# Kernel tuning notes

Hardware: AMD Instinct MI355X
Metric: run time of the kernel (lower is better)

## Reference

```python
import jax, jax.numpy as jnp
import numpy as np

DIM = 512
HEADS = 8
DIM_HEAD = 64
HIDDEN = HEADS * DIM_HEAD  # 512
B, N = 16, 4096
EPS = 1e-5


def setup_inputs() -> dict:
    key = jax.random.key(0)
    k1, k2, k3 = jax.random.split(key, 3)
    x = jax.random.normal(k1, (B, DIM, N), dtype=jnp.float32)
    # Conv1d kernel-size-1 weights stored as [out_ch, in_ch]
    w_qkv = jax.random.normal(k2, (3 * HIDDEN, DIM), dtype=jnp.float32) / np.sqrt(DIM)
    w_out = jax.random.normal(k3, (DIM, HIDDEN), dtype=jnp.float32) / np.sqrt(HIDDEN)
    b_out = jnp.zeros((DIM,), dtype=jnp.float32)
    g_out = jnp.ones((DIM,), dtype=jnp.float32)  # channel LayerNorm gamma
    return {"x": x, "w_qkv": w_qkv, "w_out": w_out, "b_out": b_out, "g_out": g_out}


def reference(x, w_qkv, w_out, b_out, g_out):
    b, c, n = x.shape
    scale = DIM_HEAD ** (-0.5)
    # 1x1 conv projection to q,k,v: [b, 3*hidden, n]
    qkv = jnp.einsum('bcn,oc->bon', x, w_qkv)
    q, k, v = jnp.split(qkv, 3, axis=1)
    rs = lambda t: t.reshape(b, HEADS, DIM_HEAD, n)  # b (m d) n -> b m d n
    q, k, v = rs(q), rs(k), rs(v)
    q = jax.nn.softmax(q, axis=2) * scale  # softmax over head-dim d
    k = jax.nn.softmax(k, axis=3)          # softmax over sequence n
    # context: k v^T outer-product summed over sequence -> [b, m, d, d]
    context = jnp.einsum('bmin,bmjn->bmij', k, v)
    # apply context to queries -> [b, m, d, n]
    out = jnp.einsum('bmij,bmin->bmjn', context, q)
    out = out.reshape(b, HIDDEN, n)  # b m d n -> b (m d) n
    # output 1x1 conv with bias
    out = jnp.einsum('bcn,oc->bon', out, w_out) + b_out[None, :, None]
    # channel LayerNorm (gamma-only, biased variance over channel axis)
    mean = out.mean(axis=1, keepdims=True)
    var = out.var(axis=1, keepdims=True)
    return (out - mean) * jax.lax.rsqrt(var + EPS) * g_out[None, :, None]
```

## Files before the change

kernel.cpp:

```cpp
#include <hip/hip_runtime.h>

#define NB 16
#define CDIM 512
#define NHEAD 8
#define DHEAD 64
#define NSEQ 4096
#define O3 1536

typedef __attribute__((ext_vector_type(8))) short short8;
typedef __attribute__((ext_vector_type(4))) float f32x4;
typedef __attribute__((ext_vector_type(4))) unsigned u32x4;
typedef __attribute__((ext_vector_type(2))) unsigned u32x2;
typedef __attribute__((ext_vector_type(4))) float fvec4;

__device__ __forceinline__ float bf2f(unsigned short u){
  union { unsigned u; float f; } v; v.u = ((unsigned)u) << 16; return v.f;
}
__device__ __forceinline__ unsigned short f2bf(float f){
  union { float f; unsigned u; } v; v.f = f;
  unsigned r = v.u + 0x7fffu + ((v.u >> 16) & 1u);
  return (unsigned short)(r >> 16);
}
__device__ __forceinline__ unsigned pack2(float a, float b){
  return (unsigned)f2bf(a) | ((unsigned)f2bf(b) << 16);
}
__device__ __forceinline__ void gld_lds16(const void* g, void* l){
  __builtin_amdgcn_global_load_lds(
      (const __attribute__((address_space(1))) unsigned*)g,
      (__attribute__((address_space(3))) unsigned*)l, 16, 0, 0);
}

__global__ __launch_bounds__(256) void k_conv_w(const float* __restrict__ w,
                                                unsigned short* __restrict__ o){
  int i = (blockIdx.x*256 + threadIdx.x)*4;
  fvec4 v = *(const fvec4*)(w + i);
  u32x2 p; p[0] = pack2(v[0], v[1]); p[1] = pack2(v[2], v[3]);
  *(u32x2*)(o + i) = p;
}

__global__ __launch_bounds__(256) void k_transpose_x(const float* __restrict__ x,
                                                     unsigned short* __restrict__ xT){
  __shared__ unsigned short tile[64][65];
  int b = blockIdx.z, c0 = blockIdx.y*64, n0 = blockIdx.x*64;
  int t = threadIdx.x;
  const float* xb = x + ((size_t)b*CDIM + c0)*NSEQ + n0;
  #pragma unroll
  for (int i=0;i<4;i++){
    int idx = t + i*256;
    int r = idx>>4, c4 = (idx&15)*4;
    fvec4 v = *(const fvec4*)(xb + (size_t)r*NSEQ + c4);
    tile[r][c4]   = f2bf(v[0]);
    tile[r][c4+1] = f2bf(v[1]);
    tile[r][c4+2] = f2bf(v[2]);
    tile[r][c4+3] = f2bf(v[3]);
  }
  __syncthreads();
  unsigned short* ob = xT + ((size_t)b*NSEQ + n0)*CDIM + c0;
  #pragma unroll
  for (int i=0;i<2;i++){
    int chunk = t + i*256;
    int r = chunk>>3, c8 = (chunk&7)*8;
    u32x4 p;
    #pragma unroll
    for (int k=0;k<4;k++)
      p[k] = (unsigned)tile[c8+2*k][r] | ((unsigned)tile[c8+2*k+1][r] << 16);
    *(u32x4*)(ob + (size_t)r*CDIM + c8) = p;
  }
}

__global__ __launch_bounds__(256) void k_gemm_kv(const unsigned short* __restrict__ A,
                                                 const unsigned short* __restrict__ Bt,
                                                 unsigned short* __restrict__ KV){
  __shared__ unsigned short As[2][128*32];
  __shared__ unsigned short Bs[2][128*32];
  int b = blockIdx.z;
  int n0 = blockIdx.x*128, o0 = blockIdx.y*128;
  const unsigned short* Bb = Bt + (size_t)b*NSEQ*CDIM;
  unsigned short* Cb = KV + (size_t)b*1024*NSEQ;
  int t = threadIdx.x, w = t>>6, l = t&63;
  int lr = l&15, kq = (l>>4)*8;
  int wr = (w>>1)*64, wc = (w&1)*64;
  f32x4 acc[4][4];
  #pragma unroll
  for (int mi=0;mi<4;mi++)
    #pragma unroll
    for (int ni=0;ni<4;ni++) acc[mi][ni] = (f32x4){0.f,0.f,0.f,0.f};
  for (int k0=0;k0<CDIM;k0+=64){
    #pragma unroll
    for (int h=0;h<2;++h){
      #pragma unroll
      for (int it=0;it<2;++it){
        int chunk = it*256 + t;
        int row = chunk>>2, kc = (chunk&3)*8;
        gld_lds16(A  + (size_t)(o0+row)*CDIM + k0 + h*32 + kc, (char*)As[h] + (size_t)chunk*16);
        gld_lds16(Bb + (size_t)(n0+row)*CDIM + k0 + h*32 + kc, (char*)Bs[h] + (size_t)chunk*16);
      }
    }
    __syncthreads();
    #pragma unroll
    for (int h=0;h<2;++h){
      short8 af[4], bfv[4];
      #pragma unroll
      for (int mi=0;mi<4;mi++) af[mi]  = *(const short8*)&As[h][(wr + mi*16 + lr)*32 + kq];
      #pragma unroll
      for (int ni=0;ni<4;ni++) bfv[ni] = *(const short8*)&Bs[h][(wc + ni*16 + lr)*32 + kq];
      #pragma unroll
      for (int mi=0;mi<4;mi++)
        #pragma unroll
        for (int ni=0;ni<4;ni++)
          acc[mi][ni] = __builtin_amdgcn_mfma_f32_16x16x32_bf16(af[mi], bfv[ni], acc[mi][ni], 0, 0, 0);
    }
    __syncthreads();
  }
  #pragma unroll
  for (int mi=0;mi<4;mi++)
    #pragma unroll
    for (int ni=0;ni<4;ni++)
      #pragma unroll
      for (int r=0;r<4;r++){
        int row = o0 + wr + mi*16 + (l>>4)*4 + r;
        int col = n0 + wc + ni*16 + lr;
        Cb[(size_t)row*NSEQ + col] = f2bf(acc[mi][ni][r]);
      }
}

#define TS 136
__global__ __launch_bounds__(256) void k_gemm_q(const unsigned short* __restrict__ A,
                                                const unsigned short* __restrict__ Bt,
                                                unsigned short* __restrict__ qsmT){
  __shared__ unsigned short smem[128*128];
  int b = blockIdx.z;
  int n0 = blockIdx.x*128, o0 = blockIdx.y*128;
  const unsigned short* Bb = Bt + (size_t)b*NSEQ*CDIM;
  int t = threadIdx.x, w = t>>6, l = t&63;
  int lr = l&15, kq = (l>>4)*8;
  int wr = (w>>1)*64, wc = (w&1)*64;
  f32x4 acc[4][4];
  #pragma unroll
  for (int mi=0;mi<4;mi++)
    #pragma unroll
    for (int ni=0;ni<4;ni++) acc[mi][ni] = (f32x4){0.f,0.f,0.f,0.f};
  for (int k0=0;k0<CDIM;k0+=64){
    #pragma unroll
    for (int h=0;h<2;++h){
      unsigned short* Ash = smem + h*4096;
      unsigned short* Bsh = smem + 8192 + h*4096;
      #pragma unroll
      for (int it=0;it<2;++it){
        int chunk = it*256 + t;
        int row = chunk>>2, kc = (chunk&3)*8;
        gld_lds16(A  + (size_t)(o0+row)*CDIM + k0 + h*32 + kc, (char*)Ash + (size_t)chunk*16);
        gld_lds16(Bb + (size_t)(n0+row)*CDIM + k0 + h*32 + kc, (char*)Bsh + (size_t)chunk*16);
      }
    }
    __syncthreads();
    #pragma unroll
    for (int h=0;h<2;++h){
      const unsigned short* Ash = smem + h*4096;
      const unsigned short* Bsh = smem + 8192 + h*4096;
      short8 af[4], bfv[4];
      #pragma unroll
      for (int mi=0;mi<4;mi++) af[mi]  = *(const short8*)&Ash[(wr + mi*16 + lr)*32 + kq];
      #pragma unroll
      for (int ni=0;ni<4;ni++) bfv[ni] = *(const short8*)&Bsh[(wc + ni*16 + lr)*32 + kq];
      #pragma unroll
      for (int mi=0;mi<4;mi++)
        #pragma unroll
        for (int ni=0;ni<4;ni++)
          acc[mi][ni] = __builtin_amdgcn_mfma_f32_16x16x32_bf16(af[mi], bfv[ni], acc[mi][ni], 0, 0, 0);
    }
    __syncthreads();
  }
  unsigned pk[4][4][2];
  #pragma unroll
  for (int ni=0;ni<4;ni++){
    float mx = -1e30f;
    #pragma unroll
    for (int mi=0;mi<4;mi++)
      #pragma unroll
      for (int r=0;r<4;r++) mx = fmaxf(mx, acc[mi][ni][r]);
    mx = fmaxf(mx, __shfl_xor(mx, 16, 64));
    mx = fmaxf(mx, __shfl_xor(mx, 32, 64));
    float s = 0.f;
    #pragma unroll
    for (int mi=0;mi<4;mi++)
      #pragma unroll
      for (int r=0;r<4;r++){
        float p = __expf(acc[mi][ni][r] - mx);
        acc[mi][ni][r] = p; s += p;
      }
    s += __shfl_xor(s, 16, 64);
    s += __shfl_xor(s, 32, 64);
    float inv = 0.125f / s;
    #pragma unroll
    for (int mi=0;mi<4;mi++){
      pk[mi][ni][0] = pack2(acc[mi][ni][0]*inv, acc[mi][ni][1]*inv);
      pk[mi][ni][1] = pack2(acc[mi][ni][2]*inv, acc[mi][ni][3]*inv);
    }
  }
  #pragma unroll
  for (int ck=0;ck<2;++ck){
    if ((w&1) == ck){
      #pragma unroll
      for (int mi=0;mi<4;mi++)
        #pragma unroll
        for (int ni=0;ni<4;ni++){
          int idx = (ni*16 + lr)*TS + wr + mi*16 + (l>>4)*4;
          u32x2 p; p[0] = pk[mi][ni][0]; p[1] = pk[mi][ni][1];
          *(u32x2*)&smem[idx] = p;
        }
    }
    __syncthreads();
    int col = t>>2, rs = (t&3)*32;
    unsigned short* dst = qsmT + ((size_t)b*NSEQ + n0 + ck*64 + col)*CDIM + o0 + rs;
    #pragma unroll
    for (int j=0;j<4;++j)
      *(u32x4*)(dst + j*8) = *(const u32x4*)&smem[col*TS + rs + j*8];
    __syncthreads();
  }
}

__global__ __launch_bounds__(256) void k_context(const unsigned short* __restrict__ KV,
                                                 float* __restrict__ ctx4,
                                                 float* __restrict__ sump){
  __shared__ unsigned short Vs[64*64];
  int m = blockIdx.x, b = blockIdx.y, ch = blockIdx.z;
  int t = threadIdx.x, w = t>>6, l = t&63;
  int lr = l&15, kq = (l>>4)*8;
  const unsigned short* kbase = KV + ((size_t)b*1024 + m*64)*NSEQ;
  const unsigned short* vbase = KV + ((size_t)b*1024 + 512 + m*64)*NSEQ;
  int irow = w*16 + lr;
  int sub = l>>4;
  int nbeg = ch*1024;
  float rsum = 0.f;
  f32x4 acc[4];
  #pragma unroll
  for (int jf=0;jf<4;++jf) acc[jf] = (f32x4){0.f,0.f,0.f,0.f};
  for (int n0=nbeg;n0<nbeg+1024;n0+=64){
    #pragma unroll
    for (int it=0;it<2;++it){
      int chunk = it*256 + t;
      int row = chunk>>3, kc = (chunk&7)*8;
      gld_lds16(vbase + (size_t)row*NSEQ + n0 + kc, (char*)Vs + (size_t)chunk*16);
    }
    __syncthreads();
    #pragma unroll
    for (int kk=0;kk<2;++kk){
      u32x4 kraw = *(const u32x4*)(kbase + (size_t)irow*NSEQ + n0 + kk*32 + kq);
      short8 af;
      #pragma unroll
      for (int c=0;c<4;++c){
        unsigned u = kraw[c];
        float f0 = __expf(bf2f((unsigned short)u));
        float f1 = __expf(bf2f((unsigned short)(u>>16)));
        rsum += f0 + f1;
        af[c*2]   = (short)f2bf(f0);
        af[c*2+1] = (short)f2bf(f1);
      }
      #pragma unroll
      for (int jf=0;jf<4;++jf){
        short8 bv = *(const short8*)&Vs[(jf*16+lr)*64 + kk*32 + kq];
        acc[jf] = __builtin_amdgcn_mfma_f32_16x16x32_bf16(af, bv, acc[jf], 0, 0, 0);
      }
    }
    __syncthreads();
  }
  rsum += __shfl_xor(rsum, 16, 64);
  rsum += __shfl_xor(rsum, 32, 64);
  size_t sbase = (((size_t)ch*NB + b)*NHEAD + m)*64;
  if (sub == 0) sump[sbase + irow] = rsum;
  float* cb = ctx4 + (((size_t)ch*NB + b)*NHEAD + m)*4096;
  #pragma unroll
  for (int jf=0;jf<4;++jf)
    #pragma unroll
    for (int r=0;r<4;++r){
      int i = w*16 + (l>>4)*4 + r;
      int j = jf*16 + lr;
      cb[i*64 + j] = acc[jf][r];
    }
}

__global__ __launch_bounds__(256) void k_weff(const float* __restrict__ ctx4,
                                              const float* __restrict__ sump,
                                              const float* __restrict__ wout,
                                              unsigned short* __restrict__ weff){
  __shared__ float cs[64][65];
  __shared__ float invZ[64];
  int m = blockIdx.x, b = blockIdx.y, z = blockIdx.z;
  int t = threadIdx.x, w = t>>6, l = t&63;
  const size_t chs = (size_t)NB*NHEAD*4096;
  const size_t sts = (size_t)NB*NHEAD*64;
  size_t sb = ((size_t)b*NHEAD + m)*64;
  if (t < 64){
    float Z = sump[sb + t] + sump[sb + sts + t]
            + sump[sb + 2*sts + t] + sump[sb + 3*sts + t];
    invZ[t] = 1.f/Z;
  }
  __syncthreads();
  const float* cb = ctx4 + ((size_t)b*NHEAD + m)*4096;
  for (int idx=t; idx<4096; idx+=256){
    int i = idx>>6;
    cs[i][idx&63] = (cb[idx] + cb[idx+chs] + cb[idx+2*chs] + cb[idx+3*chs]) * invZ[i];
  }
  __syncthreads();
  for (int oo=0;oo<32;++oo){
    int o = z*128 + w*32 + oo;
    float acc = 0.f;
    #pragma unroll
    for (int j=0;j<64;++j) acc += wout[(size_t)o*CDIM + m*64 + j] * cs[l][j];
    weff[((size_t)b*CDIM + o)*CDIM + m*64 + l] = f2bf(acc);
  }
}

__global__ __launch_bounds__(512) void k_out_ln(const unsigned short* __restrict__ Weff,
                                                const unsigned short* __restrict__ QT,
                                                const float* __restrict__ bias,
                                                const float* __restrict__ g,
                                                float* __restrict__ out){
  __shared__ unsigned short As[512*32];
  __shared__ unsigned short Bs[128*32];
  __shared__ float lnS[128], lnS2[128];
  int b = blockIdx.y, n0 = blockIdx.x*128;
  const unsigned short* Ab = Weff + (size_t)b*CDIM*CDIM;
  const unsigned short* Bb = QT + ((size_t)b*NSEQ + n0)*CDIM;
  int t = threadIdx.x, w = t>>6, l = t&63;
  int lr = l&15, kq = (l>>4)*8;
  f32x4 acc[4][8];
  #pragma unroll
  for (int mi=0;mi<4;mi++)
    #pragma unroll
    for (int ni=0;ni<8;ni++) acc[mi][ni] = (f32x4){0.f,0.f,0.f,0.f};
  for (int k0=0;k0<CDIM;k0+=32){
    #pragma unroll
    for (int it=0;it<4;++it){
      int chunk = it*512 + t;
      int row = chunk>>2, kc = (chunk&3)*8;
      gld_lds16(Ab + (size_t)row*CDIM + k0 + kc, (char*)As + (size_t)chunk*16);
    }
    {
      int row = t>>2, kc = (t&3)*8;
      gld_lds16(Bb + (size_t)row*CDIM + k0 + kc, (char*)Bs + (size_t)t*16);
    }
    __syncthreads();
    short8 af[4], bfv[8];
    #pragma unroll
    for (int mi=0;mi<4;mi++) af[mi]  = *(const short8*)&As[(w*64 + mi*16 + lr)*32 + kq];
    #pragma unroll
    for (int ni=0;ni<8;ni++) bfv[ni] = *(const short8*)&Bs[(ni*16 + lr)*32 + kq];
    #pragma unroll
    for (int mi=0;mi<4;mi++)
      #pragma unroll
      for (int ni=0;ni<8;ni++)
        acc[mi][ni] = __builtin_amdgcn_mfma_f32_16x16x32_bf16(af[mi], bfv[ni], acc[mi][ni], 0, 0, 0);
    __syncthreads();
  }
  if (t < 128){ lnS[t] = 0.f; lnS2[t] = 0.f; }
  __syncthreads();
  float ps[8], ps2[8];
  #pragma unroll
  for (int ni=0;ni<8;ni++){ ps[ni]=0.f; ps2[ni]=0.f; }
  #pragma unroll
  for (int mi=0;mi<4;mi++)
    #pragma unroll
    for (int r=0;r<4;r++){
      int row = w*64 + mi*16 + (l>>4)*4 + r;
      float bb = bias[row];
      #pragma unroll
      for (int ni=0;ni<8;ni++){
        float v = acc[mi][ni][r] + bb;
        acc[mi][ni][r] = v;
        ps[ni] += v; ps2[ni] += v*v;
      }
    }
  #pragma unroll
  for (int ni=0;ni<8;ni++){
    ps[ni]  += __shfl_xor(ps[ni], 16, 64);  ps[ni]  += __shfl_xor(ps[ni], 32, 64);
    ps2[ni] += __shfl_xor(ps2[ni], 16, 64); ps2[ni] += __shfl_xor(ps2[ni], 32, 64);
  }
  if ((l>>4) == 0){
    #pragma unroll
    for (int ni=0;ni<8;ni++){
      atomicAdd(&lnS[ni*16+lr],  ps[ni]);
      atomicAdd(&lnS2[ni*16+lr], ps2[ni]);
    }
  }
  __syncthreads();
  if (t < 128){
    float mean = lnS[t]*(1.f/512.f);
    float var  = lnS2[t]*(1.f/512.f) - mean*mean;
    lnS[t] = mean; lnS2[t] = rsqrtf(var + 1e-5f);
  }
  __syncthreads();
  float* ob = out + (size_t)b*CDIM*NSEQ + n0;
  #pragma unroll
  for (int ni=0;ni<8;ni++){
    int col = ni*16 + lr;
    float mean = lnS[col], rstd = lnS2[col];
    #pragma unroll
    for (int mi=0;mi<4;mi++)
      #pragma unroll
      for (int r=0;r<4;r++){
        int row = w*64 + mi*16 + (l>>4)*4 + r;
        ob[(size_t)row*NSEQ + col] = (acc[mi][ni][r] - mean)*rstd*g[row];
      }
  }
}

extern "C" void kernel_launch(void* const* d_in, const int* in_sizes, int n_in,
                              void* d_out, int out_size, void* d_ws, size_t ws_size,
                              hipStream_t stream){
  const float* x     = (const float*)d_in[0];
  const float* w_qkv = (const float*)d_in[1];
  const float* w_out = (const float*)d_in[2];
  const float* b_out = (const float*)d_in[3];
  const float* g_out = (const float*)d_in[4];
  float* out = (float*)d_out;
  char* ws = (char*)d_ws;

  size_t off = 0;
  unsigned short* wq_bf = (unsigned short*)(ws + off); off += (size_t)O3*CDIM*2;
  char* xT_region = ws + off;                          off += (size_t)NB*NSEQ*CDIM*2;
  unsigned short* qkv_kv = (unsigned short*)(ws + off); off += (size_t)NB*1024*NSEQ*2;
  unsigned short* qsmT   = (unsigned short*)(ws + off); off += (size_t)NB*NSEQ*CDIM*2;
  if (off > ws_size) return;
  unsigned short* xT = (unsigned short*)xT_region;
  float* sump = (float*)(xT_region);
  float* ctx4 = (float*)(xT_region + (1<<20));
  unsigned short* weff = (unsigned short*)(xT_region + (16<<20));

  k_conv_w     <<<O3*CDIM/1024, 256, 0, stream>>>(w_qkv, wq_bf);
  k_transpose_x<<<dim3(NSEQ/64, CDIM/64, NB), 256, 0, stream>>>(x, xT);
  k_gemm_kv    <<<dim3(NSEQ/128, 8, NB), 256, 0, stream>>>(wq_bf + (size_t)512*CDIM, xT, qkv_kv);
  k_gemm_q     <<<dim3(NSEQ/128, 4, NB), 256, 0, stream>>>(wq_bf, xT, qsmT);
  k_context    <<<dim3(NHEAD, NB, 4), 256, 0, stream>>>(qkv_kv, ctx4, sump);
  k_weff       <<<dim3(NHEAD, NB, 4), 256, 0, stream>>>(ctx4, sump, w_out, weff);
  k_out_ln     <<<dim3(NSEQ/128, NB), 512, 0, stream>>>(weff, qsmT, b_out, g_out, out);
}
```

Baseline: 373.4 us.

## Fuse K/V projection GEMM with exp and context accumulation per head

Merges the K/V projection GEMM and the context kernel into one kernel. Each block computes a 128-column slab of K and V for one head, applies exp and row sums to K in LDS, and accumulates K·V^T with MFMA. The goal is to stop writing and re-reading the full bf16 KV tensor (about 128 MB) to global memory. In exchange the sequence is split into 8 chunks, so the reduction in k_weff grows from 4 to 8 partials. The grid is also smaller (8x8x16 = 1024 blocks), and each block runs a second MFMA phase with extra barriers.

```diff
diff --git a/kernel.cpp b/kernel.cpp
--- a/kernel.cpp
+++ b/kernel.cpp
@@ -68,60 +68,112 @@
   }
 }
 
-__global__ __launch_bounds__(256) void k_gemm_kv(const unsigned short* __restrict__ A,
-                                                 const unsigned short* __restrict__ Bt,
-                                                 unsigned short* __restrict__ KV){
-  __shared__ unsigned short As[2][128*32];
-  __shared__ unsigned short Bs[2][128*32];
-  int b = blockIdx.z;
-  int n0 = blockIdx.x*128, o0 = blockIdx.y*128;
-  const unsigned short* Bb = Bt + (size_t)b*NSEQ*CDIM;
-  unsigned short* Cb = KV + (size_t)b*1024*NSEQ;
+#define CS 136
+__global__ __launch_bounds__(256) void k_kvctx(const unsigned short* __restrict__ wq,
+                                               const unsigned short* __restrict__ Bt,
+                                               float* __restrict__ ctx8,
+                                               float* __restrict__ sump8){
+  __shared__ char lds[35072];
+  unsigned short* AsB = (unsigned short*)lds;
+  unsigned short* BsB = (unsigned short*)(lds + 16384);
+  unsigned short* Klds = (unsigned short*)lds;
+  unsigned short* Vlds = (unsigned short*)(lds + 17408);
+  float* rsumL = (float*)(lds + 34816);
+  int ch = blockIdx.x, m = blockIdx.y, b = blockIdx.z;
   int t = threadIdx.x, w = t>>6, l = t&63;
   int lr = l&15, kq = (l>>4)*8;
   int wr = (w>>1)*64, wc = (w&1)*64;
-  f32x4 acc[4][4];
-  #pragma unroll
-  for (int mi=0;mi<4;mi++)
-    #pragma unroll
-    for (int ni=0;ni<4;ni++) acc[mi][ni] = (f32x4){0.f,0.f,0.f,0.f};
-  for (int k0=0;k0<CDIM;k0+=64){
-    #pragma unroll
-    for (int h=0;h<2;++h){
-      #pragma unroll
-      for (int it=0;it<2;++it){
-        int chunk = it*256 + t;
-        int row = chunk>>2, kc = (chunk&3)*8;
-        gld_lds16(A  + (size_t)(o0+row)*CDIM + k0 + h*32 + kc, (char*)As[h] + (size_t)chunk*16);
-        gld_lds16(Bb + (size_t)(n0+row)*CDIM + k0 + h*32 + kc, (char*)Bs[h] + (size_t)chunk*16);
-      }
-    }
-    __syncthreads();
-    #pragma unroll
-    for (int h=0;h<2;++h){
-      short8 af[4], bfv[4];
-      #pragma unroll
-      for (int mi=0;mi<4;mi++) af[mi]  = *(const short8*)&As[h][(wr + mi*16 + lr)*32 + kq];
-      #pragma unroll
-      for (int ni=0;ni<4;ni++) bfv[ni] = *(const short8*)&Bs[h][(wc + ni*16 + lr)*32 + kq];
+  const unsigned short* Ak = wq + (size_t)(512  + m*64)*CDIM;
+  const unsigned short* Av = wq + (size_t)(1024 + m*64)*CDIM;
+  if (t < 64) rsumL[t] = 0.f;
+  f32x4 cacc[4];
+  #pragma unroll
+  for (int jf=0;jf<4;++jf) cacc[jf] = (f32x4){0.f,0.f,0.f,0.f};
+
+  for (int s=0;s<4;++s){
+    const unsigned short* Bb = Bt + ((size_t)b*NSEQ + ch*512 + s*128)*CDIM;
+    f32x4 acc[4][4];
+    #pragma unroll
+    for (int mi=0;mi<4;mi++)
+      #pragma unroll
+      for (int ni=0;ni<4;ni++) acc[mi][ni] = (f32x4){0.f,0.f,0.f,0.f};
+    for (int k0=0;k0<CDIM;k0+=64){
+      #pragma unroll
+      for (int h=0;h<2;++h){
+        #pragma unroll
+        for (int it=0;it<2;++it){
+          int chunk = it*256 + t;
+          int row = chunk>>2, kc = (chunk&3)*8;
+          const unsigned short* ar = (row < 64) ? (Ak + (size_t)row*CDIM)
+                                                : (Av + (size_t)(row-64)*CDIM);
+          gld_lds16(ar + k0 + h*32 + kc, lds + (size_t)(h*512+chunk)*16);
+          gld_lds16(Bb + (size_t)row*CDIM + k0 + h*32 + kc,
+                    lds + 16384 + (size_t)(h*512+chunk)*16);
+        }
+      }
+      __syncthreads();
+      #pragma unroll
+      for (int h=0;h<2;++h){
+        short8 af[4], bfv[4];
+        #pragma unroll
+        for (int mi=0;mi<4;mi++) af[mi]  = *(const short8*)&AsB[h*4096 + (wr + mi*16 + lr)*32 + kq];
+        #pragma unroll
+        for (int ni=0;ni<4;ni++) bfv[ni] = *(const short8*)&BsB[h*4096 + (wc + ni*16 + lr)*32 + kq];
+        #pragma unroll
+        for (int mi=0;mi<4;mi++)
+          #pragma unroll
+          for (int ni=0;ni<4;ni++)
+            acc[mi][ni] = __builtin_amdgcn_mfma_f32_16x16x32_bf16(af[mi], bfv[ni], acc[mi][ni], 0, 0, 0);
+      }
+      __syncthreads();
+    }
+    if (w < 2){
       #pragma unroll
       for (int mi=0;mi<4;mi++)
         #pragma unroll
-        for (int ni=0;ni<4;ni++)
-          acc[mi][ni] = __builtin_amdgcn_mfma_f32_16x16x32_bf16(af[mi], bfv[ni], acc[mi][ni], 0, 0, 0);
-    }
-    __syncthreads();
-  }
-  #pragma unroll
-  for (int mi=0;mi<4;mi++)
-    #pragma unroll
-    for (int ni=0;ni<4;ni++)
-      #pragma unroll
-      for (int r=0;r<4;r++){
-        int row = o0 + wr + mi*16 + (l>>4)*4 + r;
-        int col = n0 + wc + ni*16 + lr;
-        Cb[(size_t)row*NSEQ + col] = f2bf(acc[mi][ni][r]);
-      }
+        for (int r=0;r<4;r++){
+          int row = mi*16 + (l>>4)*4 + r;
+          float rs = 0.f;
+          #pragma unroll
+          for (int ni=0;ni<4;ni++){
+            float e = __expf(acc[mi][ni][r]);
+            rs += e;
+            Klds[row*CS + wc + ni*16 + lr] = f2bf(e);
+          }
+          rs += __shfl_xor(rs, 1, 64); rs += __shfl_xor(rs, 2, 64);
+          rs += __shfl_xor(rs, 4, 64); rs += __shfl_xor(rs, 8, 64);
+          if (lr == 0) atomicAdd(&rsumL[row], rs);
+        }
+    } else {
+      #pragma unroll
+      for (int mi=0;mi<4;mi++)
+        #pragma unroll
+        for (int r=0;r<4;r++){
+          int row = mi*16 + (l>>4)*4 + r;
+          #pragma unroll
+          for (int ni=0;ni<4;ni++)
+            Vlds[row*CS + wc + ni*16 + lr] = f2bf(acc[mi][ni][r]);
+        }
+    }
+    __syncthreads();
+    #pragma unroll
+    for (int ks=0;ks<4;++ks){
+      short8 af = *(const short8*)&Klds[(w*16 + lr)*CS + ks*32 + kq];
+      #pragma unroll
+      for (int jf=0;jf<4;++jf){
+        short8 bv = *(const short8*)&Vlds[(jf*16 + lr)*CS + ks*32 + kq];
+        cacc[jf] = __builtin_amdgcn_mfma_f32_16x16x32_bf16(af, bv, cacc[jf], 0, 0, 0);
+      }
+    }
+    __syncthreads();
+  }
+  float* cb = ctx8 + (((size_t)ch*NB + b)*NHEAD + m)*4096;
+  #pragma unroll
+  for (int jf=0;jf<4;++jf)
+    #pragma unroll
+    for (int r=0;r<4;++r)
+      cb[(w*16 + (l>>4)*4 + r)*64 + jf*16 + lr] = cacc[jf][r];
+  if (t < 64) sump8[(((size_t)ch*NB + b)*NHEAD + m)*64 + t] = rsumL[t];
 }
 
 #define TS 136
@@ -220,68 +272,8 @@
   }
 }
 
-__global__ __launch_bounds__(256) void k_context(const unsigned short* __restrict__ KV,
-                                                 float* __restrict__ ctx4,
-                                                 float* __restrict__ sump){
-  __shared__ unsigned short Vs[64*64];
-  int m = blockIdx.x, b = blockIdx.y, ch = blockIdx.z;
-  int t = threadIdx.x, w = t>>6, l = t&63;
-  int lr = l&15, kq = (l>>4)*8;
-  const unsigned short* kbase = KV + ((size_t)b*1024 + m*64)*NSEQ;
-  const unsigned short* vbase = KV + ((size_t)b*1024 + 512 + m*64)*NSEQ;
-  int irow = w*16 + lr;
-  int sub = l>>4;
-  int nbeg = ch*1024;
-  float rsum = 0.f;
-  f32x4 acc[4];
-  #pragma unroll
-  for (int jf=0;jf<4;++jf) acc[jf] = (f32x4){0.f,0.f,0.f,0.f};
-  for (int n0=nbeg;n0<nbeg+1024;n0+=64){
-    #pragma unroll
-    for (int it=0;it<2;++it){
-      int chunk = it*256 + t;
-      int row = chunk>>3, kc = (chunk&7)*8;
-      gld_lds16(vbase + (size_t)row*NSEQ + n0 + kc, (char*)Vs + (size_t)chunk*16);
-    }
-    __syncthreads();
-    #pragma unroll
-    for (int kk=0;kk<2;++kk){
-      u32x4 kraw = *(const u32x4*)(kbase + (size_t)irow*NSEQ + n0 + kk*32 + kq);
-      short8 af;
-      #pragma unroll
-      for (int c=0;c<4;++c){
-        unsigned u = kraw[c];
-        float f0 = __expf(bf2f((unsigned short)u));
-        float f1 = __expf(bf2f((unsigned short)(u>>16)));
-        rsum += f0 + f1;
-        af[c*2]   = (short)f2bf(f0);
-        af[c*2+1] = (short)f2bf(f1);
-      }
-      #pragma unroll
-      for (int jf=0;jf<4;++jf){
-        short8 bv = *(const short8*)&Vs[(jf*16+lr)*64 + kk*32 + kq];
-        acc[jf] = __builtin_amdgcn_mfma_f32_16x16x32_bf16(af, bv, acc[jf], 0, 0, 0);
-      }
-    }
-    __syncthreads();
-  }
-  rsum += __shfl_xor(rsum, 16, 64);
-  rsum += __shfl_xor(rsum, 32, 64);
-  size_t sbase = (((size_t)ch*NB + b)*NHEAD + m)*64;
-  if (sub == 0) sump[sbase + irow] = rsum;
-  float* cb = ctx4 + (((size_t)ch*NB + b)*NHEAD + m)*4096;
-  #pragma unroll
-  for (int jf=0;jf<4;++jf)
-    #pragma unroll
-    for (int r=0;r<4;++r){
-      int i = w*16 + (l>>4)*4 + r;
-      int j = jf*16 + lr;
-      cb[i*64 + j] = acc[jf][r];
-    }
-}
-
-__global__ __launch_bounds__(256) void k_weff(const float* __restrict__ ctx4,
-                                              const float* __restrict__ sump,
+__global__ __launch_bounds__(256) void k_weff(const float* __restrict__ ctx8,
+                                              const float* __restrict__ sump8,
                                               const float* __restrict__ wout,
                                               unsigned short* __restrict__ weff){
   __shared__ float cs[64][65];
@@ -292,15 +284,19 @@
   const size_t sts = (size_t)NB*NHEAD*64;
   size_t sb = ((size_t)b*NHEAD + m)*64;
   if (t < 64){
-    float Z = sump[sb + t] + sump[sb + sts + t]
-            + sump[sb + 2*sts + t] + sump[sb + 3*sts + t];
+    float Z = 0.f;
+    #pragma unroll
+    for (int c=0;c<8;++c) Z += sump8[sb + c*sts + t];
     invZ[t] = 1.f/Z;
   }
   __syncthreads();
-  const float* cb = ctx4 + ((size_t)b*NHEAD + m)*4096;
+  const float* cb = ctx8 + ((size_t)b*NHEAD + m)*4096;
   for (int idx=t; idx<4096; idx+=256){
     int i = idx>>6;
-    cs[i][idx&63] = (cb[idx] + cb[idx+chs] + cb[idx+2*chs] + cb[idx+3*chs]) * invZ[i];
+    float v = 0.f;
+    #pragma unroll
+    for (int c=0;c<8;++c) v += cb[idx + c*chs];
+    cs[i][idx&63] = v * invZ[i];
   }
   __syncthreads();
   for (int oo=0;oo<32;++oo){
@@ -419,20 +415,18 @@
 
   size_t off = 0;
   unsigned short* wq_bf = (unsigned short*)(ws + off); off += (size_t)O3*CDIM*2;
-  char* xT_region = ws + off;                          off += (size_t)NB*NSEQ*CDIM*2;
-  unsigned short* qkv_kv = (unsigned short*)(ws + off); off += (size_t)NB*1024*NSEQ*2;
-  unsigned short* qsmT   = (unsigned short*)(ws + off); off += (size_t)NB*NSEQ*CDIM*2;
+  unsigned short* xT    = (unsigned short*)(ws + off); off += (size_t)NB*NSEQ*CDIM*2;
+  char* scratch = ws + off;                            off += (size_t)NB*1024*NSEQ*2;
+  unsigned short* qsmT  = (unsigned short*)(ws + off); off += (size_t)NB*NSEQ*CDIM*2;
   if (off > ws_size) return;
-  unsigned short* xT = (unsigned short*)xT_region;
-  float* sump = (float*)(xT_region);
-  float* ctx4 = (float*)(xT_region + (1<<20));
-  unsigned short* weff = (unsigned short*)(xT_region + (16<<20));
+  float* sump8 = (float*)(scratch);
+  float* ctx8  = (float*)(scratch + (1<<20));
+  unsigned short* weff = (unsigned short*)(scratch + (20<<20));
 
   k_conv_w     <<<O3*CDIM/1024, 256, 0, stream>>>(w_qkv, wq_bf);
   k_transpose_x<<<dim3(NSEQ/64, CDIM/64, NB), 256, 0, stream>>>(x, xT);
-  k_gemm_kv    <<<dim3(NSEQ/128, 8, NB), 256, 0, stream>>>(wq_bf + (size_t)512*CDIM, xT, qkv_kv);
+  k_kvctx      <<<dim3(8, NHEAD, NB), 256, 0, stream>>>(wq_bf, xT, ctx8, sump8);
   k_gemm_q     <<<dim3(NSEQ/128, 4, NB), 256, 0, stream>>>(wq_bf, xT, qsmT);
-  k_context    <<<dim3(NHEAD, NB, 4), 256, 0, stream>>>(qkv_kv, ctx4, sump);
-  k_weff       <<<dim3(NHEAD, NB, 4), 256, 0, stream>>>(ctx4, sump, w_out, weff);
+  k_weff       <<<dim3(NHEAD, NB, 4), 256, 0, stream>>>(ctx8, sump8, w_out, weff);
   k_out_ln     <<<dim3(NSEQ/128, NB), 512, 0, stream>>>(weff, qsmT, b_out, g_out, out);
 }
```

Result: slower. 445.2 us (+19.2%).

## Double-buffer K-slices in QKV projection GEMMs to overlap loads with MFMA

Applied to the files above, without the earlier changes.

Changes the kv and q projection GEMM main loops from loading a 64-wide K chunk and then computing on it into a ping-pong pipeline over 32-wide K slices. The next slice is prefetched into the alternate LDS buffer while MFMAs run on the current one, with one barrier per step. The goal is to hide global-to-LDS latency behind compute. In exchange it doubles the number of barriers and loop iterations, and correctness relies on the async LDS load having landed before the barrier.

```diff
diff --git a/kernel.cpp b/kernel.cpp
--- a/kernel.cpp
+++ b/kernel.cpp
@@ -85,32 +85,33 @@
   for (int mi=0;mi<4;mi++)
     #pragma unroll
     for (int ni=0;ni<4;ni++) acc[mi][ni] = (f32x4){0.f,0.f,0.f,0.f};
-  for (int k0=0;k0<CDIM;k0+=64){
-    #pragma unroll
-    for (int h=0;h<2;++h){
-      #pragma unroll
-      for (int it=0;it<2;++it){
-        int chunk = it*256 + t;
-        int row = chunk>>2, kc = (chunk&3)*8;
-        gld_lds16(A  + (size_t)(o0+row)*CDIM + k0 + h*32 + kc, (char*)As[h] + (size_t)chunk*16);
-        gld_lds16(Bb + (size_t)(n0+row)*CDIM + k0 + h*32 + kc, (char*)Bs[h] + (size_t)chunk*16);
-      }
-    }
-    __syncthreads();
-    #pragma unroll
-    for (int h=0;h<2;++h){
-      short8 af[4], bfv[4];
-      #pragma unroll
-      for (int mi=0;mi<4;mi++) af[mi]  = *(const short8*)&As[h][(wr + mi*16 + lr)*32 + kq];
-      #pragma unroll
-      for (int ni=0;ni<4;ni++) bfv[ni] = *(const short8*)&Bs[h][(wc + ni*16 + lr)*32 + kq];
-      #pragma unroll
-      for (int mi=0;mi<4;mi++)
-        #pragma unroll
-        for (int ni=0;ni<4;ni++)
-          acc[mi][ni] = __builtin_amdgcn_mfma_f32_16x16x32_bf16(af[mi], bfv[ni], acc[mi][ni], 0, 0, 0);
-    }
-    __syncthreads();
+  auto STAGE = [&](int k0, int buf){
+    #pragma unroll
+    for (int it=0;it<2;++it){
+      int chunk = it*256 + t;
+      int row = chunk>>2, kc = (chunk&3)*8;
+      gld_lds16(A  + (size_t)(o0+row)*CDIM + k0 + kc, (char*)As[buf] + (size_t)chunk*16);
+      gld_lds16(Bb + (size_t)(n0+row)*CDIM + k0 + kc, (char*)Bs[buf] + (size_t)chunk*16);
+    }
+  };
+  STAGE(0, 0);
+  __syncthreads();
+  int cur = 0;
+  #pragma unroll 2
+  for (int k0=0;k0<CDIM;k0+=32){
+    if (k0+32 < CDIM) STAGE(k0+32, cur^1);
+    short8 af[4], bfv[4];
+    #pragma unroll
+    for (int mi=0;mi<4;mi++) af[mi]  = *(const short8*)&As[cur][(wr + mi*16 + lr)*32 + kq];
+    #pragma unroll
+    for (int ni=0;ni<4;ni++) bfv[ni] = *(const short8*)&Bs[cur][(wc + ni*16 + lr)*32 + kq];
+    #pragma unroll
+    for (int mi=0;mi<4;mi++)
+      #pragma unroll
+      for (int ni=0;ni<4;ni++)
+        acc[mi][ni] = __builtin_amdgcn_mfma_f32_16x16x32_bf16(af[mi], bfv[ni], acc[mi][ni], 0, 0, 0);
+    __syncthreads();
+    cur ^= 1;
   }
   #pragma unroll
   for (int mi=0;mi<4;mi++)
@@ -140,36 +141,37 @@
   for (int mi=0;mi<4;mi++)
     #pragma unroll
     for (int ni=0;ni<4;ni++) acc[mi][ni] = (f32x4){0.f,0.f,0.f,0.f};
-  for (int k0=0;k0<CDIM;k0+=64){
-    #pragma unroll
-    for (int h=0;h<2;++h){
-      unsigned short* Ash = smem + h*4096;
-      unsigned short* Bsh = smem + 8192 + h*4096;
-      #pragma unroll
-      for (int it=0;it<2;++it){
-        int chunk = it*256 + t;
-        int row = chunk>>2, kc = (chunk&3)*8;
-        gld_lds16(A  + (size_t)(o0+row)*CDIM + k0 + h*32 + kc, (char*)Ash + (size_t)chunk*16);
-        gld_lds16(Bb + (size_t)(n0+row)*CDIM + k0 + h*32 + kc, (char*)Bsh + (size_t)chunk*16);
-      }
-    }
-    __syncthreads();
-    #pragma unroll
-    for (int h=0;h<2;++h){
-      const unsigned short* Ash = smem + h*4096;
-      const unsigned short* Bsh = smem + 8192 + h*4096;
-      short8 af[4], bfv[4];
-      #pragma unroll
-      for (int mi=0;mi<4;mi++) af[mi]  = *(const short8*)&Ash[(wr + mi*16 + lr)*32 + kq];
-      #pragma unroll
-      for (int ni=0;ni<4;ni++) bfv[ni] = *(const short8*)&Bsh[(wc + ni*16 + lr)*32 + kq];
-      #pragma unroll
-      for (int mi=0;mi<4;mi++)
-        #pragma unroll
-        for (int ni=0;ni<4;ni++)
-          acc[mi][ni] = __builtin_amdgcn_mfma_f32_16x16x32_bf16(af[mi], bfv[ni], acc[mi][ni], 0, 0, 0);
-    }
-    __syncthreads();
+  auto STAGE = [&](int k0, int buf){
+    unsigned short* Ash = smem + buf*4096;
+    unsigned short* Bsh = smem + 8192 + buf*4096;
+    #pragma unroll
+    for (int it=0;it<2;++it){
+      int chunk = it*256 + t;
+      int row = chunk>>2, kc = (chunk&3)*8;
+      gld_lds16(A  + (size_t)(o0+row)*CDIM + k0 + kc, (char*)Ash + (size_t)chunk*16);
+      gld_lds16(Bb + (size_t)(n0+row)*CDIM + k0 + kc, (char*)Bsh + (size_t)chunk*16);
+    }
+  };
+  STAGE(0, 0);
+  __syncthreads();
+  int cur = 0;
+  #pragma unroll 2
+  for (int k0=0;k0<CDIM;k0+=32){
+    if (k0+32 < CDIM) STAGE(k0+32, cur^1);
+    const unsigned short* Ash = smem + cur*4096;
+    const unsigned short* Bsh = smem + 8192 + cur*4096;
+    short8 af[4], bfv[4];
+    #pragma unroll
+    for (int mi=0;mi<4;mi++) af[mi]  = *(const short8*)&Ash[(wr + mi*16 + lr)*32 + kq];
+    #pragma unroll
+    for (int ni=0;ni<4;ni++) bfv[ni] = *(const short8*)&Bsh[(wc + ni*16 + lr)*32 + kq];
+    #pragma unroll
+    for (int mi=0;mi<4;mi++)
+      #pragma unroll
+      for (int ni=0;ni<4;ni++)
+        acc[mi][ni] = __builtin_amdgcn_mfma_f32_16x16x32_bf16(af[mi], bfv[ni], acc[mi][ni], 0, 0, 0);
+    __syncthreads();
+    cur ^= 1;
   }
   unsigned pk[4][4][2];
   #pragma unroll
```

Measured after the change: 382.2 us. +2.4%, slower.
